# Kernel optimization log

Measured on AMD Instinct MI355X. Metric: run time of the kernel, lower is better.

Reference implementation:

```python
import jax, jax.numpy as jnp
import numpy as np

D_MODEL = 512
NUM_HEADS = 8
D_QKV = D_MODEL // NUM_HEADS  # 64
CAPACITY = 2  # EUNN tunable-style rotation layers per step
B = 2
L = 256


def setup_inputs() -> dict:
    key = jax.random.key(0)
    ks = jax.random.split(key, 16)
    f = jnp.float32
    x_q = jax.random.normal(ks[0], (B, L, D_MODEL), f)
    x_k = jax.random.normal(ks[1], (B, L, D_MODEL), f)
    x_v = jax.random.normal(ks[2], (B, L, D_MODEL), f)
    mask = jnp.zeros((B, 1, L, L), f)
    s = 1.0 / np.sqrt(D_MODEL).astype(np.float32)
    Wq = jax.random.normal(ks[3], (D_MODEL, D_MODEL), f) * s
    Wk = jax.random.normal(ks[4], (D_MODEL, D_MODEL), f) * s
    Wv = jax.random.normal(ks[5], (D_MODEL, D_MODEL), f) * s
    Wo = jax.random.normal(ks[6], (D_MODEL, D_MODEL), f) * s
    bq = jnp.zeros((D_MODEL,), f); bk = jnp.zeros((D_MODEL,), f)
    bv = jnp.zeros((D_MODEL,), f); bo = jnp.zeros((D_MODEL,), f)
    pi = np.float32(np.pi)
    theta = jax.random.uniform(ks[7], (NUM_HEADS, CAPACITY, D_QKV // 2), f, -pi, pi)
    phi = jax.random.uniform(ks[8], (NUM_HEADS, CAPACITY, D_QKV // 2), f, -pi, pi)
    sw = 1.0 / np.sqrt(D_QKV).astype(np.float32)
    Win_re = jax.random.normal(ks[9], (NUM_HEADS, D_QKV, D_QKV), f) * sw
    Win_im = jax.random.normal(ks[10], (NUM_HEADS, D_QKV, D_QKV), f) * sw
    rnn_bias = jax.random.normal(ks[11], (NUM_HEADS, D_QKV), f) * 0.01
    return dict(x_q=x_q, x_k=x_k, x_v=x_v, mask=mask, Wq=Wq, bq=bq, Wk=Wk, bk=bk,
                Wv=Wv, bv=bv, Wo=Wo, bo=bo, theta=theta, phi=phi,
                Win_re=Win_re, Win_im=Win_im, rnn_bias=rnn_bias)


def _apply_unitary(h, theta, phi):
    # h: [B,H,Q,d] complex64. EUNN unitary = product of Givens-rotation layers,
    # alternating even pairings (0,1),(2,3),.. and odd pairings via roll.
    for c in range(theta.shape[1]):
        if c % 2 == 1:
            h = jnp.roll(h, -1, axis=-1)
        sh = h.shape
        hp = h.reshape(sh[:-1] + (sh[-1] // 2, 2))
        a, b = hp[..., 0], hp[..., 1]
        cs = jnp.cos(theta[:, c, :])[None, :, None, :]
        sn = jnpp_sin = jnp.sin(theta[:, c, :])[None, :, None, :]
        ph = jnp.exp(1j * phi[:, c, :].astype(jnp.complex64))[None, :, None, :]
        na = cs * a - (sn * ph) * b
        nb = (sn * jnp.conj(ph)) * a + cs * b
        h = jnp.stack([na, nb], axis=-1).reshape(sh)
        if c % 2 == 1:
            h = jnp.roll(h, 1, axis=-1)
    return h


def _modrelu(z, b):
    m = jnp.abs(z)
    scale = jax.nn.relu(m + b) / (m + 1e-5)
    return z * scale.astype(z.dtype)


def _forward(x_q, x_k, x_v, mask, Wq, bq, Wk, bk, Wv, bv, Wo, bo,
             theta, phi, Win_re, Win_im, rnn_bias):
    Bm, Lq, _ = x_q.shape
    def heads(x):
        return x.reshape(Bm, -1, NUM_HEADS, D_QKV).transpose(0, 2, 1, 3)
    q = heads(x_q @ Wq + bq)   # [B,H,Lq,d]
    k = heads(x_k @ Wk + bk)   # [B,H,Lk,d]
    v = heads(x_v @ Wv + bv)   # [B,H,Lk,d]
    logits = jnp.einsum('bhqd,bhkd->bhqk', q, k) / jnp.sqrt(jnp.float32(D_QKV))
    logits = logits - jnp.where(mask == 1.0, jnp.inf, mask)
    attn = jax.nn.softmax(logits, axis=-1)  # [B,H,Lq,Lk]
    Win = (Win_re + 1j * Win_im).astype(jnp.complex64)  # [H,d,d]
    bb = rnn_bias[None, :, None, :]
    def step(h, xs):
        a_t, v_t = xs                              # [B,H,Q], [B,H,d]
        x_t = a_t[..., None] * v_t[:, :, None, :]  # [B,H,Q,d] streamed weighted value
        wx = jnp.einsum('bhqd,hde->bhqe', x_t.astype(jnp.complex64), Win)
        return _modrelu(_apply_unitary(h, theta, phi) + wx, bb), None
    h0 = jnp.zeros((Bm, NUM_HEADS, Lq, D_QKV), jnp.complex64)
    xs = (attn.transpose(3, 0, 1, 2), v.transpose(2, 0, 1, 3))
    hT, _ = jax.lax.scan(step, h0, xs)
    rnn_out = jnp.real(hT)  # [B,H,Lq,d] -- TF takes final RNN state, real part
    out = rnn_out.transpose(0, 2, 1, 3).reshape(Bm, Lq, D_MODEL) @ Wo + bo
    return out, attn


def reference(x_q, x_k, x_v, mask, Wq, bq, Wk, bk, Wv, bv, Wo, bo,
              theta, phi, Win_re, Win_im, rnn_bias):
    return _forward(x_q, x_k, x_v, mask, Wq, bq, Wk, bk, Wv, bv, Wo, bo,
                    theta, phi, Win_re, Win_im, rnn_bias)
```

## Files before the change

kernel.cpp:

```cpp
#include <hip/hip_runtime.h>
#include <math.h>

#define NB 2
#define NL 256
#define DM 512
#define NH 8
#define DQ 64

typedef float v2f __attribute__((ext_vector_type(2)));

#if __has_builtin(__builtin_elementwise_fma)
__device__ __forceinline__ v2f fmav(v2f a, v2f b, v2f c) {
    return __builtin_elementwise_fma(a, b, c);
}
#else
__device__ __forceinline__ v2f fmav(v2f a, v2f b, v2f c) {
    v2f r; r.x = fmaf(a.x, b.x, c.x); r.y = fmaf(a.y, b.y, c.y); return r;
}
#endif
__device__ __forceinline__ v2f swapv(v2f a) {
    return __builtin_shufflevector(a, a, 1, 0);
}

__global__ __launch_bounds__(256) void qkv_gemm(
    const float* __restrict__ xq, const float* __restrict__ xk,
    const float* __restrict__ xv,
    const float* __restrict__ Wq, const float* __restrict__ Wk,
    const float* __restrict__ Wv,
    const float* __restrict__ bq, const float* __restrict__ bk,
    const float* __restrict__ bv,
    const float* __restrict__ Wre, const float* __restrict__ Wim,
    float* __restrict__ q, float* __restrict__ kT, float2* __restrict__ u)
{
    int z = blockIdx.z;
    const float* X = (z == 0) ? xq : (z == 1) ? xk : xv;
    const float* W = (z == 0) ? Wq : (z == 1) ? Wk : Wv;
    const float* bias = (z == 0) ? bq : (z == 1) ? bk : bv;

    __shared__ float As[32][33];
    __shared__ float Bs[32][68];

    int tid = threadIdx.x;
    int tx = tid & 15, ty = tid >> 4;
    int m0 = blockIdx.y * 32, n0 = blockIdx.x * 64;

    int ar = tid >> 3, ac4 = (tid & 7) * 4;
    int br = tid >> 4, bc4 = (tid & 15) * 4;
    const float* Aptr = X + (m0 + ar) * 512 + ac4;
    const float* Bptr0 = W + br * 512 + n0 + bc4;
    const float* Bptr1 = W + (br + 16) * 512 + n0 + bc4;

    float acc[2][4] = {};

    float4 aR = *(const float4*)(Aptr);
    float4 bR0 = *(const float4*)(Bptr0);
    float4 bR1 = *(const float4*)(Bptr1);

    for (int k0 = 0; k0 < 512; k0 += 32) {
        As[ac4 + 0][ar] = aR.x; As[ac4 + 1][ar] = aR.y;
        As[ac4 + 2][ar] = aR.z; As[ac4 + 3][ar] = aR.w;
        *(float4*)&Bs[br][bc4] = bR0;
        *(float4*)&Bs[br + 16][bc4] = bR1;
        __syncthreads();

        if (k0 + 32 < 512) {
            aR  = *(const float4*)(Aptr + k0 + 32);
            bR0 = *(const float4*)(Bptr0 + (k0 + 32) * 512);
            bR1 = *(const float4*)(Bptr1 + (k0 + 32) * 512);
        }

        #pragma unroll
        for (int kk = 0; kk < 32; kk++) {
            float a0 = As[kk][ty * 2 + 0];
            float a1 = As[kk][ty * 2 + 1];
            float4 bb = *(const float4*)&Bs[kk][tx * 4];
            acc[0][0] += a0 * bb.x; acc[0][1] += a0 * bb.y;
            acc[0][2] += a0 * bb.z; acc[0][3] += a0 * bb.w;
            acc[1][0] += a1 * bb.x; acc[1][1] += a1 * bb.y;
            acc[1][2] += a1 * bb.z; acc[1][3] += a1 * bb.w;
        }
        __syncthreads();
    }

    if (z < 2) {
        float* O = (z == 0) ? q : kT;
        #pragma unroll
        for (int i = 0; i < 2; i++) {
            int m = m0 + ty * 2 + i;
            int b = m >> 8, l = m & 255;
            #pragma unroll
            for (int j = 0; j < 4; j++) {
                int n = n0 + tx * 4 + j;
                int h = n >> 6, d = n & 63;
                float val = acc[i][j] + bias[n];
                if (z == 1)
                    O[((b * NH + h) * DQ + d) * NL + l] = val;
                else
                    O[((b * NH + h) * NL + l) * DQ + d] = val;
            }
        }
    } else {
        int h = blockIdx.x;
        int b = m0 >> 8;
        #pragma unroll
        for (int i = 0; i < 2; i++)
            #pragma unroll
            for (int j = 0; j < 4; j++)
                Bs[ty * 2 + i][tx * 4 + j] = acc[i][j] + bias[n0 + tx * 4 + j];
        __syncthreads();

        int r0 = ty * 2, c4 = tx * 4;
        float ur[2][4] = {}, ui[2][4] = {};
        const float* wr = Wre + h * 4096 + c4;
        const float* wi = Wim + h * 4096 + c4;
        #pragma unroll 4
        for (int d = 0; d < 64; d++) {
            float v0 = Bs[r0][d];
            float v1 = Bs[r0 + 1][d];
            float4 wre = *(const float4*)(wr + d * 64);
            float4 wim = *(const float4*)(wi + d * 64);
            ur[0][0] += v0 * wre.x; ur[0][1] += v0 * wre.y;
            ur[0][2] += v0 * wre.z; ur[0][3] += v0 * wre.w;
            ui[0][0] += v0 * wim.x; ui[0][1] += v0 * wim.y;
            ui[0][2] += v0 * wim.z; ui[0][3] += v0 * wim.w;
            ur[1][0] += v1 * wre.x; ur[1][1] += v1 * wre.y;
            ur[1][2] += v1 * wre.z; ur[1][3] += v1 * wre.w;
            ui[1][0] += v1 * wim.x; ui[1][1] += v1 * wim.y;
            ui[1][2] += v1 * wim.z; ui[1][3] += v1 * wim.w;
        }
        #pragma unroll
        for (int i = 0; i < 2; i++) {
            int l = (m0 & 255) + r0 + i;
            float2* up = u + ((size_t)(b * NH + h) * NL + l) * DQ + c4;
            #pragma unroll
            for (int j = 0; j < 4; j++)
                up[j] = make_float2(ur[i][j], ui[i][j]);
        }
    }
}

__device__ __forceinline__ float rot_up2(float x) {
    int v = __builtin_amdgcn_mov_dpp(__float_as_int(x), 0x134, 0xF, 0xF, true);
    v = __builtin_amdgcn_mov_dpp(v, 0x134, 0xF, 0xF, true);
    return __int_as_float(v);
}
__device__ __forceinline__ float rot_dn2(float x) {
    int v = __builtin_amdgcn_mov_dpp(__float_as_int(x), 0x13C, 0xF, 0xF, true);
    v = __builtin_amdgcn_mov_dpp(v, 0x13C, 0xF, 0xF, true);
    return __int_as_float(v);
}

__global__ __launch_bounds__(256) void rnn_kernel(
    const float* __restrict__ q, const float* __restrict__ kT,
    const float* __restrict__ mask, float* __restrict__ attn_o,
    const float2* __restrict__ u,
    const float* __restrict__ theta, const float* __restrict__ phi,
    const float* __restrict__ rnn_bias, float* __restrict__ rnn_out)
{
    int tid = threadIdx.x;
    int wv = tid >> 6;
    int lane = tid & 63;

    int qg = blockIdx.x & 31;
    int h  = (blockIdx.x >> 5) & 7;
    int b  = blockIdx.x >> 8;

    __shared__ float sp[2608];
    __shared__ float arow[8 * 256];

    {
        float* qs   = sp;
        float* lg   = sp + 512;
        float* redm = sp + 512 + 2080;
        float* reds = redm + 8;

        ((float2*)qs)[tid] =
            ((const float2*)(q + ((size_t)(b * NH + h) * NL + qg * 8) * DQ))[tid];
        __syncthreads();

        const float* kp = kT + (size_t)((b * NH + h) * DQ) * NL + tid;
        float acc[8] = {};
        #pragma unroll
        for (int d4 = 0; d4 < 16; d4++) {
            float kv0 = kp[(d4 * 4 + 0) * NL];
            float kv1 = kp[(d4 * 4 + 1) * NL];
            float kv2 = kp[(d4 * 4 + 2) * NL];
            float kv3 = kp[(d4 * 4 + 3) * NL];
            #pragma unroll
            for (int j = 0; j < 8; j++) {
                const float4 qv = *(const float4*)&qs[j * 64 + d4 * 4];
                acc[j] += qv.x * kv0 + qv.y * kv1 + qv.z * kv2 + qv.w * kv3;
            }
        }
        #pragma unroll
        for (int j = 0; j < 8; j++) {
            float mv = mask[(size_t)(b * NL + qg * 8 + j) * NL + tid];
            acc[j] = acc[j] * 0.125f - ((mv == 1.0f) ? INFINITY : mv);
            lg[j * 260 + tid] = acc[j];
        }
        __syncthreads();
        #pragma unroll
        for (int jj = 0; jj < 2; jj++) {
            int j = wv * 2 + jj;
            float v0 = lg[j * 260 + lane],       v1 = lg[j * 260 + 64 + lane];
            float v2 = lg[j * 260 + 128 + lane], v3 = lg[j * 260 + 192 + lane];
            float mx = fmaxf(fmaxf(v0, v1), fmaxf(v2, v3));
            #pragma unroll
            for (int o = 32; o; o >>= 1) mx = fmaxf(mx, __shfl_xor(mx, o, 64));
            float s = __expf(v0 - mx) + __expf(v1 - mx) +
                      __expf(v2 - mx) + __expf(v3 - mx);
            #pragma unroll
            for (int o = 32; o; o >>= 1) s += __shfl_xor(s, o, 64);
            if (lane == 0) { redm[j] = mx; reds[j] = s; }
        }
        __syncthreads();
        #pragma unroll
        for (int j = 0; j < 8; j++) {
            float p = __expf(acc[j] - redm[j]) * __builtin_amdgcn_rcpf(reds[j]);
            attn_o[((size_t)(b * NH + h) * NL + qg * 8 + j) * NL + tid] = p;
            arow[j * 256 + tid] = p;
        }
        __syncthreads();
    }

    int par = lane & 1;
    int p = lane >> 1;
    int rec = blockIdx.x * 8 + wv * 2 + par;
    int qi = rec & 255;

    const float* tb = theta + h * 64;
    const float* pb = phi + h * 64;

    float th0 = tb[p], ph0 = pb[p];
    float c0 = cosf(th0), s0 = sinf(th0);
    float cp0 = cosf(ph0), sp0 = sinf(ph0);
    float W0ar = -s0 * cp0, W0ai = -s0 * sp0;
    float W0br =  s0 * cp0, W0bi = -s0 * sp0;

    float th1 = tb[32 + p], ph1 = pb[32 + p];
    float c1 = cosf(th1), s1 = sinf(th1);
    float W1ar = -s1 * cosf(ph1), W1ai = -s1 * sinf(ph1);

    int pm = (p + 31) & 31;
    float th1m = tb[32 + pm], ph1m = pb[32 + pm];
    float c1m = cosf(th1m), s1m = sinf(th1m);
    float W1br = s1m * cosf(ph1m), W1bi = -s1m * sinf(ph1m);

    float bias0 = rnn_bias[h * 64 + 2 * p];
    float bias1 = rnn_bias[h * 64 + 2 * p + 1];

    v2f c0v  = {c0, c0},   c1v  = {c1, c1},   c1mv = {c1m, c1m};
    v2f W0arV = {W0ar, W0ar}, W0aiN = {-W0ai, W0ai};
    v2f W0brV = {W0br, W0br}, W0biN = {-W0bi, W0bi};
    v2f W1arV = {W1ar, W1ar}, W1aiN = {-W1ai, W1ai};
    v2f W1brV = {W1br, W1br}, W1biN = {-W1bi, W1bi};

    const float* arc = arow + (wv * 2 + par) * 256;
    const float4* up4 = (const float4*)(u + (size_t)((b * NH + h) * NL) * DQ) + p;

    v2f e0 = {0.f, 0.f}, e1 = {0.f, 0.f};
    #pragma unroll 8
    for (int t = 0; t < 256; t++) {
        float4 uu = up4[t * 32];
        float a_t = arc[t];
        v2f atv = {a_t, a_t};
        v2f u0 = {uu.x, uu.y}, u1 = {uu.z, uu.w};

        v2f na = fmav(c0v, e0, fmav(W0arV, e1, W0aiN * swapv(e1)));
        v2f nb = fmav(c0v, e1, fmav(W0brV, e0, W0biN * swapv(e0)));

        v2f f1, f2;
        f1.x = rot_up2(na.x); f1.y = rot_up2(na.y);
        f2.x = rot_dn2(nb.x); f2.y = rot_dn2(nb.y);

        v2f z1 = fmav(c1v, nb, fmav(W1arV, f1, fmav(W1aiN, swapv(f1), atv * u1)));
        v2f z0 = fmav(c1mv, na, fmav(W1brV, f2, fmav(W1biN, swapv(f2), atv * u0)));

        float mm0 = z0.x * z0.x + z0.y * z0.y;
        float m0 = __builtin_amdgcn_sqrtf(mm0);
        float sc0 = fmaxf(m0 + bias0, 0.f) * __builtin_amdgcn_rcpf(m0 + 1e-5f);
        v2f sc0v = {sc0, sc0};
        e0 = z0 * sc0v;

        float mm1 = z1.x * z1.x + z1.y * z1.y;
        float m1 = __builtin_amdgcn_sqrtf(mm1);
        float sc1 = fmaxf(m1 + bias1, 0.f) * __builtin_amdgcn_rcpf(m1 + 1e-5f);
        v2f sc1v = {sc1, sc1};
        e1 = z1 * sc1v;
    }

    float2 o = make_float2(e0.x, e1.x);
    *(float2*)&rnn_out[(size_t)(b * NL + qi) * DM + h * DQ + 2 * p] = o;
}

__global__ __launch_bounds__(256) void out_gemm(
    const float* __restrict__ A, const float* __restrict__ W,
    const float* __restrict__ bias, float* __restrict__ C)
{
    __shared__ float As[32][17];
    __shared__ float Bs[32][68];

    int tid = threadIdx.x;
    int tx = tid & 15, ty = tid >> 4;
    int m0 = blockIdx.y * 16, n0 = blockIdx.x * 64;

    int ar = tid >> 4, ac2 = (tid & 15) * 2;
    int br = tid >> 4, bc4 = (tid & 15) * 4;
    const float* Aptr = A + (m0 + ar) * 512 + ac2;
    const float* Bptr0 = W + br * 512 + n0 + bc4;
    const float* Bptr1 = W + (br + 16) * 512 + n0 + bc4;

    float acc[4] = {};

    float2 aR = *(const float2*)(Aptr);
    float4 bR0 = *(const float4*)(Bptr0);
    float4 bR1 = *(const float4*)(Bptr1);

    for (int k0 = 0; k0 < 512; k0 += 32) {
        As[ac2 + 0][ar] = aR.x; As[ac2 + 1][ar] = aR.y;
        *(float4*)&Bs[br][bc4] = bR0;
        *(float4*)&Bs[br + 16][bc4] = bR1;
        __syncthreads();

        if (k0 + 32 < 512) {
            aR  = *(const float2*)(Aptr + k0 + 32);
            bR0 = *(const float4*)(Bptr0 + (k0 + 32) * 512);
            bR1 = *(const float4*)(Bptr1 + (k0 + 32) * 512);
        }

        #pragma unroll
        for (int kk = 0; kk < 32; kk++) {
            float a = As[kk][ty];
            float4 bb = *(const float4*)&Bs[kk][tx * 4];
            acc[0] += a * bb.x; acc[1] += a * bb.y;
            acc[2] += a * bb.z; acc[3] += a * bb.w;
        }
        __syncthreads();
    }

    int m = m0 + ty;
    #pragma unroll
    for (int j = 0; j < 4; j++) {
        int n = n0 + tx * 4 + j;
        C[m * 512 + n] = acc[j] + bias[n];
    }
}

extern "C" void kernel_launch(void* const* d_in, const int* in_sizes, int n_in,
                              void* d_out, int out_size, void* d_ws, size_t ws_size,
                              hipStream_t stream)
{
    const float* x_q  = (const float*)d_in[0];
    const float* x_k  = (const float*)d_in[1];
    const float* x_v  = (const float*)d_in[2];
    const float* mask = (const float*)d_in[3];
    const float* Wq   = (const float*)d_in[4];
    const float* bq   = (const float*)d_in[5];
    const float* Wk   = (const float*)d_in[6];
    const float* bk   = (const float*)d_in[7];
    const float* Wv   = (const float*)d_in[8];
    const float* bv   = (const float*)d_in[9];
    const float* Wo   = (const float*)d_in[10];
    const float* bo   = (const float*)d_in[11];
    const float* theta= (const float*)d_in[12];
    const float* phi  = (const float*)d_in[13];
    const float* Wre  = (const float*)d_in[14];
    const float* Wim  = (const float*)d_in[15];
    const float* rb   = (const float*)d_in[16];

    float* ws = (float*)d_ws;
    float*  q_ws    = ws;
    float*  kT_ws   = ws + 262144;
    float2* u_ws    = (float2*)(ws + 524288);
    float*  rnn_o   = ws + 1048576;

    float* out_o  = (float*)d_out;
    float* attn_o = out_o + NB * NL * DM;

    qkv_gemm<<<dim3(8, 16, 3), 256, 0, stream>>>(
        x_q, x_k, x_v, Wq, Wk, Wv, bq, bk, bv, Wre, Wim,
        q_ws, kT_ws, u_ws);

    rnn_kernel<<<dim3(512), 256, 0, stream>>>(
        q_ws, kT_ws, mask, attn_o, u_ws, theta, phi, rb, rnn_o);

    out_gemm<<<dim3(8, 32), 256, 0, stream>>>(rnn_o, Wo, bo, out_o);
}
```

Measured before the change: 188.4 us.

## Map one RNN state element per lane and double rnn_kernel grid

Each lane in the recurrent scan now owns a single complex element of the 64-wide state. Previously a lane held a pair, and two query rows were interleaved per wave. Each block now handles 4 query rows instead of 8, so the grid doubles to 1024 blocks. Givens rotations use single-step DPP swap and rotate with a per-lane select, which shortens the serial per-step dependency chain and raises parallelism. In exchange, the logits and softmax work per block is duplicated across more blocks, and per-step u loads become narrower float2 reads.

After: 188.5 us. No clear change (+0.0%).

```diff
diff --git a/kernel.cpp b/kernel.cpp
--- a/kernel.cpp
+++ b/kernel.cpp
@@ -139,15 +139,14 @@
     }
 }
 
-__device__ __forceinline__ float rot_up2(float x) {
-    int v = __builtin_amdgcn_mov_dpp(__float_as_int(x), 0x134, 0xF, 0xF, true);
-    v = __builtin_amdgcn_mov_dpp(v, 0x134, 0xF, 0xF, true);
-    return __int_as_float(v);
-}
-__device__ __forceinline__ float rot_dn2(float x) {
-    int v = __builtin_amdgcn_mov_dpp(__float_as_int(x), 0x13C, 0xF, 0xF, true);
-    v = __builtin_amdgcn_mov_dpp(v, 0x13C, 0xF, 0xF, true);
-    return __int_as_float(v);
+__device__ __forceinline__ float dpp_swap1(float x) {
+    return __int_as_float(__builtin_amdgcn_mov_dpp(__float_as_int(x), 0xB1, 0xF, 0xF, true));
+}
+__device__ __forceinline__ float dpp_rol1(float x) {
+    return __int_as_float(__builtin_amdgcn_mov_dpp(__float_as_int(x), 0x134, 0xF, 0xF, true));
+}
+__device__ __forceinline__ float dpp_ror1(float x) {
+    return __int_as_float(__builtin_amdgcn_mov_dpp(__float_as_int(x), 0x13C, 0xF, 0xF, true));
 }
 
 __global__ __launch_bounds__(256) void rnn_kernel(
@@ -157,29 +156,26 @@
     const float* __restrict__ theta, const float* __restrict__ phi,
     const float* __restrict__ rnn_bias, float* __restrict__ rnn_out)
 {
-    int tid = threadIdx.x;
-    int wv = tid >> 6;
+    int tid  = threadIdx.x;
+    int wv   = tid >> 6;
     int lane = tid & 63;
 
-    int qg = blockIdx.x & 31;
-    int h  = (blockIdx.x >> 5) & 7;
-    int b  = blockIdx.x >> 8;
-
-    __shared__ float sp[2608];
-    __shared__ float arow[8 * 256];
+    int blk = blockIdx.x;
+    int qg  = blk & 63;
+    int h   = (blk >> 6) & 7;
+    int b   = blk >> 9;
+
+    __shared__ float qs[256];
+    __shared__ float lg[4 * 260];
+    __shared__ float redm[4], reds[4];
+    __shared__ float arow[4 * 256];
 
     {
-        float* qs   = sp;
-        float* lg   = sp + 512;
-        float* redm = sp + 512 + 2080;
-        float* reds = redm + 8;
-
-        ((float2*)qs)[tid] =
-            ((const float2*)(q + ((size_t)(b * NH + h) * NL + qg * 8) * DQ))[tid];
+        qs[tid] = q[((size_t)(b * NH + h) * NL + qg * 4) * DQ + tid];
         __syncthreads();
 
         const float* kp = kT + (size_t)((b * NH + h) * DQ) * NL + tid;
-        float acc[8] = {};
+        float acc[4] = {};
         #pragma unroll
         for (int d4 = 0; d4 < 16; d4++) {
             float kv0 = kp[(d4 * 4 + 0) * NL];
@@ -187,21 +183,20 @@
             float kv2 = kp[(d4 * 4 + 2) * NL];
             float kv3 = kp[(d4 * 4 + 3) * NL];
             #pragma unroll
-            for (int j = 0; j < 8; j++) {
+            for (int j = 0; j < 4; j++) {
                 const float4 qv = *(const float4*)&qs[j * 64 + d4 * 4];
                 acc[j] += qv.x * kv0 + qv.y * kv1 + qv.z * kv2 + qv.w * kv3;
             }
         }
         #pragma unroll
-        for (int j = 0; j < 8; j++) {
-            float mv = mask[(size_t)(b * NL + qg * 8 + j) * NL + tid];
+        for (int j = 0; j < 4; j++) {
+            float mv = mask[(size_t)(b * NL + qg * 4 + j) * NL + tid];
             acc[j] = acc[j] * 0.125f - ((mv == 1.0f) ? INFINITY : mv);
             lg[j * 260 + tid] = acc[j];
         }
         __syncthreads();
-        #pragma unroll
-        for (int jj = 0; jj < 2; jj++) {
-            int j = wv * 2 + jj;
+        {
+            int j = wv;
             float v0 = lg[j * 260 + lane],       v1 = lg[j * 260 + 64 + lane];
             float v2 = lg[j * 260 + 128 + lane], v3 = lg[j * 260 + 192 + lane];
             float mx = fmaxf(fmaxf(v0, v1), fmaxf(v2, v3));
@@ -215,82 +210,71 @@
         }
         __syncthreads();
         #pragma unroll
-        for (int j = 0; j < 8; j++) {
+        for (int j = 0; j < 4; j++) {
             float p = __expf(acc[j] - redm[j]) * __builtin_amdgcn_rcpf(reds[j]);
-            attn_o[((size_t)(b * NH + h) * NL + qg * 8 + j) * NL + tid] = p;
+            attn_o[((size_t)(b * NH + h) * NL + qg * 4 + j) * NL + tid] = p;
             arow[j * 256 + tid] = p;
         }
         __syncthreads();
     }
 
-    int par = lane & 1;
-    int p = lane >> 1;
-    int rec = blockIdx.x * 8 + wv * 2 + par;
-    int qi = rec & 255;
+    int d = lane;
+    bool odd = d & 1;
 
     const float* tb = theta + h * 64;
     const float* pb = phi + h * 64;
 
-    float th0 = tb[p], ph0 = pb[p];
+    int i0 = d >> 1;
+    float th0 = tb[i0], ph0 = pb[i0];
     float c0 = cosf(th0), s0 = sinf(th0);
-    float cp0 = cosf(ph0), sp0 = sinf(ph0);
-    float W0ar = -s0 * cp0, W0ai = -s0 * sp0;
-    float W0br =  s0 * cp0, W0bi = -s0 * sp0;
-
-    float th1 = tb[32 + p], ph1 = pb[32 + p];
+    float W0r = (odd ? s0 : -s0) * cosf(ph0);
+    float W0i = -s0 * sinf(ph0);
+
+    int i1 = odd ? (d >> 1) : (((d + 62) & 63) >> 1);
+    float th1 = tb[32 + i1], ph1 = pb[32 + i1];
     float c1 = cosf(th1), s1 = sinf(th1);
-    float W1ar = -s1 * cosf(ph1), W1ai = -s1 * sinf(ph1);
-
-    int pm = (p + 31) & 31;
-    float th1m = tb[32 + pm], ph1m = pb[32 + pm];
-    float c1m = cosf(th1m), s1m = sinf(th1m);
-    float W1br = s1m * cosf(ph1m), W1bi = -s1m * sinf(ph1m);
-
-    float bias0 = rnn_bias[h * 64 + 2 * p];
-    float bias1 = rnn_bias[h * 64 + 2 * p + 1];
-
-    v2f c0v  = {c0, c0},   c1v  = {c1, c1},   c1mv = {c1m, c1m};
-    v2f W0arV = {W0ar, W0ar}, W0aiN = {-W0ai, W0ai};
-    v2f W0brV = {W0br, W0br}, W0biN = {-W0bi, W0bi};
-    v2f W1arV = {W1ar, W1ar}, W1aiN = {-W1ai, W1ai};
-    v2f W1brV = {W1br, W1br}, W1biN = {-W1bi, W1bi};
-
-    const float* arc = arow + (wv * 2 + par) * 256;
-    const float4* up4 = (const float4*)(u + (size_t)((b * NH + h) * NL) * DQ) + p;
-
-    v2f e0 = {0.f, 0.f}, e1 = {0.f, 0.f};
+    float W1r = (odd ? -s1 : s1) * cosf(ph1);
+    float W1i = -s1 * sinf(ph1);
+
+    float biasv = rnn_bias[h * 64 + d];
+
+    v2f c0v = {c0, c0}, c1v = {c1, c1};
+    v2f W0rV = {W0r, W0r}, W0iN = {-W0i, W0i};
+    v2f W1rV = {W1r, W1r}, W1iN = {-W1i, W1i};
+
+    const float* arc = arow + wv * 256;
+    const float2* up = u + (size_t)((b * NH + h) * NL) * DQ + d;
+
+    v2f e = {0.f, 0.f};
     #pragma unroll 8
     for (int t = 0; t < 256; t++) {
-        float4 uu = up4[t * 32];
+        float2 uu = up[t * 64];
         float a_t = arc[t];
         v2f atv = {a_t, a_t};
-        v2f u0 = {uu.x, uu.y}, u1 = {uu.z, uu.w};
-
-        v2f na = fmav(c0v, e0, fmav(W0arV, e1, W0aiN * swapv(e1)));
-        v2f nb = fmav(c0v, e1, fmav(W0brV, e0, W0biN * swapv(e0)));
-
-        v2f f1, f2;
-        f1.x = rot_up2(na.x); f1.y = rot_up2(na.y);
-        f2.x = rot_dn2(nb.x); f2.y = rot_dn2(nb.y);
-
-        v2f z1 = fmav(c1v, nb, fmav(W1arV, f1, fmav(W1aiN, swapv(f1), atv * u1)));
-        v2f z0 = fmav(c1mv, na, fmav(W1brV, f2, fmav(W1biN, swapv(f2), atv * u0)));
-
-        float mm0 = z0.x * z0.x + z0.y * z0.y;
-        float m0 = __builtin_amdgcn_sqrtf(mm0);
-        float sc0 = fmaxf(m0 + bias0, 0.f) * __builtin_amdgcn_rcpf(m0 + 1e-5f);
-        v2f sc0v = {sc0, sc0};
-        e0 = z0 * sc0v;
-
-        float mm1 = z1.x * z1.x + z1.y * z1.y;
-        float m1 = __builtin_amdgcn_sqrtf(mm1);
-        float sc1 = fmaxf(m1 + bias1, 0.f) * __builtin_amdgcn_rcpf(m1 + 1e-5f);
-        v2f sc1v = {sc1, sc1};
-        e1 = z1 * sc1v;
-    }
-
-    float2 o = make_float2(e0.x, e1.x);
-    *(float2*)&rnn_out[(size_t)(b * NL + qi) * DM + h * DQ + 2 * p] = o;
+        v2f uv = {uu.x, uu.y};
+
+        v2f p0;
+        p0.x = dpp_swap1(e.x); p0.y = dpp_swap1(e.y);
+        v2f g = fmav(c0v, e, fmav(W0rV, p0, W0iN * swapv(p0)));
+
+        v2f rl, rr;
+        rl.x = dpp_rol1(g.x); rl.y = dpp_rol1(g.y);
+        rr.x = dpp_ror1(g.x); rr.y = dpp_ror1(g.y);
+        v2f p1;
+        p1.x = odd ? rl.x : rr.x;
+        p1.y = odd ? rl.y : rr.y;
+
+        v2f z = fmav(c1v, g, fmav(W1rV, p1, fmav(W1iN, swapv(p1), atv * uv)));
+
+        float mm = z.x * z.x + z.y * z.y;
+        float m = __builtin_amdgcn_sqrtf(mm);
+        float sc = fmaxf(m + biasv, 0.f) * __builtin_amdgcn_rcpf(m + 1e-5f);
+        v2f scv = {sc, sc};
+        e = z * scv;
+    }
+
+    int qi = qg * 4 + wv;
+    rnn_out[(size_t)(b * NL + qi) * DM + h * DQ + d] = e.x;
 }
 
 __global__ __launch_bounds__(256) void out_gemm(
@@ -381,7 +365,7 @@
         x_q, x_k, x_v, Wq, Wk, Wv, bq, bk, bv, Wre, Wim,
         q_ws, kT_ws, u_ws);
 
-    rnn_kernel<<<dim3(512), 256, 0, stream>>>(
+    rnn_kernel<<<dim3(1024), 256, 0, stream>>>(
         q_ws, kT_ws, mask, attn_o, u_ws, theta, phi, rb, rnn_o);
 
     out_gemm<<<dim3(8, 32), 256, 0, stream>>>(rnn_o, Wo, bo, out_o);
```
